# Kernel optimization log

Hardware: AMD Instinct MI355X
Metric: run time of the kernel (lower is better)

The kernel has to match this reference:

```python
import jax, jax.numpy as jnp
import numpy as np

N_SITES = 64   # lattice sites
BOND = 32      # virtual bond dimension D
PHYS = 2       # physical (spin) dimension
BATCH = 32768  # Monte Carlo samples


def spin_to_occupancy(s):
    # spins in {-1,+1} -> physical indices in {0,1}
    return ((s + 1) // 2).astype(jnp.int32)


def setup_inputs() -> dict:
    key = jax.random.key(0)
    k1, k2, k3, k4 = jax.random.split(key, 4)
    # site tensors: boundary sites have bond dim 1, interior sites are (PHYS, D, D)
    t_first = jax.random.uniform(k1, (PHYS, 1, BOND), dtype=jnp.float32)
    t_mid = jax.random.uniform(k2, (N_SITES - 2, PHYS, BOND, BOND), dtype=jnp.float32)
    t_last = jax.random.uniform(k3, (PHYS, BOND, 1), dtype=jnp.float32)
    bits = jax.random.randint(k4, (BATCH, N_SITES), 0, 2)
    x = (2 * bits - 1).astype(jnp.int32)  # spins +-1
    return {"t_first": t_first, "t_mid": t_mid, "t_last": t_last, "x": x}


def reference(t_first, t_mid, t_last, x):
    idx = spin_to_occupancy(x)  # (B, n_sites)
    # first site: left bond = 1, so state = t_first[idx0, 0, :]  (B, D)
    state = t_first[idx[:, 0], 0, :]

    # interior sites: sequential chain of gather + batched mat-vec
    def step(state, xs):
        T, i = xs            # T: (PHYS, D, D), i: (B,)
        mats = T[i]          # (B, D, D) gather by physical index
        return jnp.einsum('bi,bij->bj', state, mats), None

    state, _ = jax.lax.scan(step, state, (t_mid, idx[:, 1:-1].T))

    # last site: right bond = 1
    amps = jnp.einsum('bi,bi->b', state, t_last[idx[:, -1], :, 0])  # (B,)
    return jnp.log(amps)
```

## Files before the change

kernel.cpp:

```cpp
#include <hip/hip_runtime.h>
#include <math.h>

#define N_MID 62
#define NPAIR 31
#define BATCH 32768

typedef float f32x4 __attribute__((ext_vector_type(4)));
typedef unsigned int u32x2 __attribute__((ext_vector_type(2)));
typedef unsigned int u32x4 __attribute__((ext_vector_type(4)));

__device__ __forceinline__ long mklong(unsigned a, unsigned b) {
    u32x2 t = {a, b};
    return __builtin_bit_cast(long, t);
}
__device__ __forceinline__ unsigned pack_fp8x4(float a, float b, float c, float d) {
    int r = __builtin_amdgcn_cvt_pk_fp8_f32(a, b, 0, false);
    r = __builtin_amdgcn_cvt_pk_fp8_f32(c, d, r, true);
    return (unsigned)r;
}

__global__ __launch_bounds__(64) void prefix_kernel(const float* __restrict__ t_mid,
                                                    unsigned* __restrict__ wsP) {
    __shared__ float M1s[1024], M2s[1024];
    const int l = threadIdx.x, q = l >> 4, m = l & 15;
    const int i = blockIdx.x >> 2, v = blockIdx.x & 3;

    const float4* s1 = (const float4*)(t_mid + (size_t)((2 * i) * 2 + (v & 1)) * 1024);
    const float4* s2 = (const float4*)(t_mid + (size_t)((2 * i + 1) * 2 + (v >> 1)) * 1024);
    #pragma unroll
    for (int c = 0; c < 4; ++c) {
        ((float4*)M1s)[c * 64 + l] = s1[c * 64 + l];
        ((float4*)M2s)[c * 64 + l] = s2[c * 64 + l];
    }
    __syncthreads();

    float colv[2][32];
    #pragma unroll
    for (int t = 0; t < 2; ++t)
        #pragma unroll
        for (int mm = 0; mm < 32; ++mm)
            colv[t][mm] = M2s[mm * 32 + 16 * t + m];

    float o0[8], o1[8];
    #pragma unroll
    for (int j = 0; j < 8; ++j) {
        int a = 16 * (j >> 2) + 4 * q + (j & 3);
        float acc0 = 0.f, acc1 = 0.f;
        #pragma unroll
        for (int mm = 0; mm < 32; ++mm) {
            float r = M1s[a * 32 + mm];
            acc0 = fmaf(r, colv[0][mm], acc0);
            acc1 = fmaf(r, colv[1][mm], acc1);
        }
        o0[j] = acc0;
        o1[j] = acc1;
    }

    u32x4 outw;
    outw[0] = pack_fp8x4(o0[0], o0[1], o0[2], o0[3]);
    outw[1] = pack_fp8x4(o0[4], o0[5], o0[6], o0[7]);
    outw[2] = pack_fp8x4(o1[0], o1[1], o1[2], o1[3]);
    outw[3] = pack_fp8x4(o1[4], o1[5], o1[6], o1[7]);
    ((u32x4*)wsP)[blockIdx.x * 64 + l] = outw;
}

__global__ __launch_bounds__(256, 2) void mps_mfma_kernel(
    const float* __restrict__ t_first,
    const float* __restrict__ t_last,
    const int*   __restrict__ x,
    const unsigned* __restrict__ wsP,
    float* __restrict__ out)
{
    const int tid  = threadIdx.x;
    const int w    = tid >> 6;
    const int l    = tid & 63;
    const int q    = l >> 4;
    const int e    = l & 15;
    const int base = (blockIdx.x * 4 + w) * 16;

    unsigned long long mrot;
    {
        const int4* xr = (const int4*)(x + (size_t)(base + e) * 64 + 16 * q);
        unsigned chunk = 0;
        #pragma unroll
        for (int c = 0; c < 4; ++c) {
            int4 vv = xr[c];
            chunk |= (unsigned)(vv.x > 0) << (4 * c + 0);
            chunk |= (unsigned)(vv.y > 0) << (4 * c + 1);
            chunk |= (unsigned)(vv.z > 0) << (4 * c + 2);
            chunk |= (unsigned)(vv.w > 0) << (4 * c + 3);
        }
        unsigned sh = chunk << ((q & 1) * 16);
        unsigned lo = (q < 2) ? sh : 0u;
        unsigned hi = (q >= 2) ? sh : 0u;
        lo |= (unsigned)__shfl_xor((int)lo, 16);
        lo |= (unsigned)__shfl_xor((int)lo, 32);
        hi |= (unsigned)__shfl_xor((int)hi, 16);
        hi |= (unsigned)__shfl_xor((int)hi, 32);
        unsigned long long mask = ((unsigned long long)hi << 32) | lo;
        const float* tf = t_first + ((mask & 1ull) ? 32 : 0);
        mrot = mask >> 1;
        (void)tf;
    }

    float st[8];
    {
        const float* tf = t_first + ((x[(size_t)(base + e) * 64] > 0) ? 32 : 0);
        #pragma unroll
        for (int j = 0; j < 8; ++j)
            st[j] = tf[16 * (j >> 2) + 4 * q + (j & 3)];
    }
    unsigned Bd0 = pack_fp8x4(st[0], st[1], st[2], st[3]);
    unsigned Bd1 = pack_fp8x4(st[4], st[5], st[6], st[7]);

    int expsum = 0;
    const f32x4 cz = {0.f, 0.f, 0.f, 0.f};

    const u32x4* W = (const u32x4*)wsP + l;
    u32x4 Q0[4], Q1[4];
    #pragma unroll
    for (int v = 0; v < 4; ++v) Q0[v] = W[v * 64];
    #pragma unroll
    for (int v = 0; v < 4; ++v) Q1[v] = W[(4 + v) * 64];

    auto step = [&](u32x4* Q, const u32x4* pf) {
        unsigned vl = (unsigned)mrot & 3u;
        mrot >>= 2;

        f32x4 y0 = cz, y1 = cz;
        #pragma unroll
        for (int v = 0; v < 4; ++v) {
            long A0 = mklong(Q[v][0], Q[v][1]);
            long A1 = mklong(Q[v][2], Q[v][3]);
            bool sel = (vl == (unsigned)v);
            long u = mklong(sel ? Bd0 : 0u, sel ? Bd1 : 0u);
            y0 = __builtin_amdgcn_mfma_f32_16x16x32_fp8_fp8(A0, u, y0, 0, 0, 0);
            y1 = __builtin_amdgcn_mfma_f32_16x16x32_fp8_fp8(A1, u, y1, 0, 0, 0);
        }

        if (pf) {
            #pragma unroll
            for (int v = 0; v < 4; ++v) Q[v] = pf[v * 64];
        }

        #pragma unroll
        for (int r = 0; r < 4; ++r) { st[r] = y0[r]; st[4 + r] = y1[r]; }

        float mx = st[0];
        #pragma unroll
        for (int j = 1; j < 8; ++j) mx = fmaxf(mx, st[j]);
        mx = fmaxf(mx, __shfl_xor(mx, 16));
        mx = fmaxf(mx, __shfl_xor(mx, 32));
        int ex = (int)((__float_as_uint(mx) >> 23) & 0xFF) - 127;
        float sc = __uint_as_float((unsigned)(127 - ex) << 23);
        #pragma unroll
        for (int j = 0; j < 8; ++j) st[j] *= sc;
        expsum += ex;

        Bd0 = pack_fp8x4(st[0], st[1], st[2], st[3]);
        Bd1 = pack_fp8x4(st[4], st[5], st[6], st[7]);
    };

    const u32x4* pf = W + 8 * 64;
    for (int k = 0; k < 15; ++k) {
        step(Q0, pf);
        step(Q1, (k < 14) ? pf + 4 * 64 : nullptr);
        pf += 8 * 64;
    }
    step(Q0, nullptr);

    const float* tl = t_last + ((mrot & 1ull) ? 32 : 0);
    float amp = 0.f;
    #pragma unroll
    for (int j = 0; j < 8; ++j)
        amp = fmaf(st[j], tl[16 * (j >> 2) + 4 * q + (j & 3)], amp);
    amp += __shfl_xor(amp, 16);
    amp += __shfl_xor(amp, 32);

    if (l < 16)
        out[base + l] = logf(amp) + 0.69314718055994531f * (float)expsum;
}

extern "C" void kernel_launch(void* const* d_in, const int* in_sizes, int n_in,
                              void* d_out, int out_size, void* d_ws, size_t ws_size,
                              hipStream_t stream) {
    const float* t_first = (const float*)d_in[0];
    const float* t_mid   = (const float*)d_in[1];
    const float* t_last  = (const float*)d_in[2];
    const int*   x       = (const int*)d_in[3];
    float* out           = (float*)d_out;

    unsigned* wsP = (unsigned*)d_ws;

    hipLaunchKernelGGL(prefix_kernel, dim3(NPAIR * 4), dim3(64), 0, stream, t_mid, wsP);
    hipLaunchKernelGGL(mps_mfma_kernel, dim3(BATCH / 64), dim3(256), 0, stream,
                       t_first, t_last, x, wsP, out);
}
```

Baseline: 78.49 us.

## Use 16x16x128 scaled FP8 MFMA per step with permlane-swapped B operand

Each chain step previously issued eight 16x16x32 FP8 MFMAs, four per output half. It now issues two 16x16x128 f8f6f4 scaled MFMAs, with unit scales, by stacking the four two-site variants along K. The prefix kernel writes its output in a layout that matches the new A operand. Each lane gathers the state vector for its variant slot with permlane16/32 swaps, and the max reduction also uses these swaps instead of shuffles. The goal is to shorten the serial dependency chain per step, at the cost of extra cross-lane data movement and a layout that must match exactly.

```diff
diff --git a/kernel.cpp b/kernel.cpp
--- a/kernel.cpp
+++ b/kernel.cpp
@@ -1,28 +1,45 @@
 #include <hip/hip_runtime.h>
 #include <math.h>
 
-#define N_MID 62
 #define NPAIR 31
 #define BATCH 32768
 
 typedef float f32x4 __attribute__((ext_vector_type(4)));
+typedef int   i32x8 __attribute__((ext_vector_type(8)));
 typedef unsigned int u32x2 __attribute__((ext_vector_type(2)));
 typedef unsigned int u32x4 __attribute__((ext_vector_type(4)));
 
-__device__ __forceinline__ long mklong(unsigned a, unsigned b) {
-    u32x2 t = {a, b};
-    return __builtin_bit_cast(long, t);
-}
 __device__ __forceinline__ unsigned pack_fp8x4(float a, float b, float c, float d) {
     int r = __builtin_amdgcn_cvt_pk_fp8_f32(a, b, 0, false);
     r = __builtin_amdgcn_cvt_pk_fp8_f32(c, d, r, true);
     return (unsigned)r;
 }
 
+__device__ __forceinline__ void lane_swap16(unsigned a, unsigned& ev, unsigned& od) {
+#if __has_builtin(__builtin_amdgcn_permlane16_swap)
+    auto r = __builtin_amdgcn_permlane16_swap((int)a, (int)a, false, false);
+    ev = (unsigned)r[0]; od = (unsigned)r[1];
+#else
+    unsigned p = (unsigned)__shfl_xor((int)a, 16);
+    bool hi = (threadIdx.x >> 4) & 1;
+    ev = hi ? p : a; od = hi ? a : p;
+#endif
+}
+__device__ __forceinline__ void lane_swap32(unsigned a, unsigned& lo, unsigned& hi) {
+#if __has_builtin(__builtin_amdgcn_permlane32_swap)
+    auto r = __builtin_amdgcn_permlane32_swap((int)a, (int)a, false, false);
+    lo = (unsigned)r[0]; hi = (unsigned)r[1];
+#else
+    unsigned p = (unsigned)__shfl_xor((int)a, 32);
+    bool up = (threadIdx.x & 32) != 0;
+    lo = up ? p : a; hi = up ? a : p;
+#endif
+}
+
 __global__ __launch_bounds__(64) void prefix_kernel(const float* __restrict__ t_mid,
                                                     unsigned* __restrict__ wsP) {
     __shared__ float M1s[1024], M2s[1024];
-    const int l = threadIdx.x, q = l >> 4, m = l & 15;
+    const int l = threadIdx.x, h = l >> 4, m = l & 15;
     const int i = blockIdx.x >> 2, v = blockIdx.x & 3;
 
     const float4* s1 = (const float4*)(t_mid + (size_t)((2 * i) * 2 + (v & 1)) * 1024);
@@ -44,7 +61,7 @@
     float o0[8], o1[8];
     #pragma unroll
     for (int j = 0; j < 8; ++j) {
-        int a = 16 * (j >> 2) + 4 * q + (j & 3);
+        int a = 16 * (j >> 2) + 4 * h + (j & 3);
         float acc0 = 0.f, acc1 = 0.f;
         #pragma unroll
         for (int mm = 0; mm < 32; ++mm) {
@@ -56,13 +73,57 @@
         o1[j] = acc1;
     }
 
-    u32x4 outw;
-    outw[0] = pack_fp8x4(o0[0], o0[1], o0[2], o0[3]);
-    outw[1] = pack_fp8x4(o0[4], o0[5], o0[6], o0[7]);
-    outw[2] = pack_fp8x4(o1[0], o1[1], o1[2], o1[3]);
-    outw[3] = pack_fp8x4(o1[4], o1[5], o1[6], o1[7]);
-    ((u32x4*)wsP)[blockIdx.x * 64 + l] = outw;
-}
+    unsigned* dst0 = wsP + (((size_t)blockIdx.x * 2 + 0) * 16 + m) * 8 + h * 2;
+    u32x2 w0 = {pack_fp8x4(o0[0], o0[1], o0[2], o0[3]),
+                pack_fp8x4(o0[4], o0[5], o0[6], o0[7])};
+    *(u32x2*)dst0 = w0;
+    unsigned* dst1 = wsP + (((size_t)blockIdx.x * 2 + 1) * 16 + m) * 8 + h * 2;
+    u32x2 w1 = {pack_fp8x4(o1[0], o1[1], o1[2], o1[3]),
+                pack_fp8x4(o1[4], o1[5], o1[6], o1[7])};
+    *(u32x2*)dst1 = w1;
+}
+
+#define MPS_STEP(QQ, PF) do {                                                 \
+    unsigned vl = (unsigned)mrot & 3u; mrot >>= 2;                            \
+    unsigned E0, O0, E1, O1;                                                  \
+    lane_swap16(Bd0, E0, O0); lane_swap16(Bd1, E1, O1);                       \
+    unsigned g0, g1, g2, g3, g4, g5, g6, g7;                                  \
+    lane_swap32(E0, g0, g4); lane_swap32(E1, g1, g5);                         \
+    lane_swap32(O0, g2, g6); lane_swap32(O1, g3, g7);                         \
+    bool selq = (vl == (unsigned)q);                                          \
+    i32x8 Bv;                                                                 \
+    Bv[0] = selq ? (int)g0 : 0; Bv[1] = selq ? (int)g1 : 0;                   \
+    Bv[2] = selq ? (int)g2 : 0; Bv[3] = selq ? (int)g3 : 0;                   \
+    Bv[4] = selq ? (int)g4 : 0; Bv[5] = selq ? (int)g5 : 0;                   \
+    Bv[6] = selq ? (int)g6 : 0; Bv[7] = selq ? (int)g7 : 0;                   \
+    i32x8 A0v, A1v;                                                           \
+    A0v[0]=(int)QQ[0][0]; A0v[1]=(int)QQ[0][1]; A0v[2]=(int)QQ[0][2]; A0v[3]=(int)QQ[0][3]; \
+    A0v[4]=(int)QQ[1][0]; A0v[5]=(int)QQ[1][1]; A0v[6]=(int)QQ[1][2]; A0v[7]=(int)QQ[1][3]; \
+    A1v[0]=(int)QQ[2][0]; A1v[1]=(int)QQ[2][1]; A1v[2]=(int)QQ[2][2]; A1v[3]=(int)QQ[2][3]; \
+    A1v[4]=(int)QQ[3][0]; A1v[5]=(int)QQ[3][1]; A1v[6]=(int)QQ[3][2]; A1v[7]=(int)QQ[3][3]; \
+    const u32x4* pf_ = (PF);                                                  \
+    if (pf_) { QQ[0] = pf_[0]; QQ[1] = pf_[1]; QQ[2] = pf_[32]; QQ[3] = pf_[33]; } \
+    f32x4 y0 = __builtin_amdgcn_mfma_scale_f32_16x16x128_f8f6f4(              \
+        A0v, Bv, cz, 0, 0, 0, 0x7f7f7f7f, 0, 0x7f7f7f7f);                     \
+    f32x4 y1 = __builtin_amdgcn_mfma_scale_f32_16x16x128_f8f6f4(              \
+        A1v, Bv, cz, 0, 0, 0, 0x7f7f7f7f, 0, 0x7f7f7f7f);                     \
+    _Pragma("unroll")                                                         \
+    for (int r = 0; r < 4; ++r) { st[r] = y0[r]; st[4 + r] = y1[r]; }         \
+    float mx = fmaxf(fmaxf(fmaxf(st[0], st[1]), fmaxf(st[2], st[3])),         \
+                     fmaxf(fmaxf(st[4], st[5]), fmaxf(st[6], st[7])));        \
+    { unsigned a_, b_;                                                        \
+      lane_swap16(__float_as_uint(mx), a_, b_);                               \
+      mx = fmaxf(__uint_as_float(a_), __uint_as_float(b_));                   \
+      lane_swap32(__float_as_uint(mx), a_, b_);                               \
+      mx = fmaxf(__uint_as_float(a_), __uint_as_float(b_)); }                 \
+    int ex = (int)((__float_as_uint(mx) >> 23) & 0xFF) - 127;                 \
+    float sc = __uint_as_float((unsigned)(127 - ex) << 23);                   \
+    _Pragma("unroll")                                                         \
+    for (int j = 0; j < 8; ++j) st[j] *= sc;                                  \
+    expsum += ex;                                                             \
+    Bd0 = pack_fp8x4(st[0], st[1], st[2], st[3]);                             \
+    Bd1 = pack_fp8x4(st[4], st[5], st[6], st[7]);                             \
+} while (0)
 
 __global__ __launch_bounds__(256, 2) void mps_mfma_kernel(
     const float* __restrict__ t_first,
@@ -98,9 +159,7 @@
         hi |= (unsigned)__shfl_xor((int)hi, 16);
         hi |= (unsigned)__shfl_xor((int)hi, 32);
         unsigned long long mask = ((unsigned long long)hi << 32) | lo;
-        const float* tf = t_first + ((mask & 1ull) ? 32 : 0);
         mrot = mask >> 1;
-        (void)tf;
     }
 
     float st[8];
@@ -116,58 +175,18 @@
     int expsum = 0;
     const f32x4 cz = {0.f, 0.f, 0.f, 0.f};
 
-    const u32x4* W = (const u32x4*)wsP + l;
+    const u32x4* Wl = (const u32x4*)wsP + (q * 64 + e * 2);
     u32x4 Q0[4], Q1[4];
-    #pragma unroll
-    for (int v = 0; v < 4; ++v) Q0[v] = W[v * 64];
-    #pragma unroll
-    for (int v = 0; v < 4; ++v) Q1[v] = W[(4 + v) * 64];
-
-    auto step = [&](u32x4* Q, const u32x4* pf) {
-        unsigned vl = (unsigned)mrot & 3u;
-        mrot >>= 2;
-
-        f32x4 y0 = cz, y1 = cz;
-        #pragma unroll
-        for (int v = 0; v < 4; ++v) {
-            long A0 = mklong(Q[v][0], Q[v][1]);
-            long A1 = mklong(Q[v][2], Q[v][3]);
-            bool sel = (vl == (unsigned)v);
-            long u = mklong(sel ? Bd0 : 0u, sel ? Bd1 : 0u);
-            y0 = __builtin_amdgcn_mfma_f32_16x16x32_fp8_fp8(A0, u, y0, 0, 0, 0);
-            y1 = __builtin_amdgcn_mfma_f32_16x16x32_fp8_fp8(A1, u, y1, 0, 0, 0);
-        }
-
-        if (pf) {
-            #pragma unroll
-            for (int v = 0; v < 4; ++v) Q[v] = pf[v * 64];
-        }
-
-        #pragma unroll
-        for (int r = 0; r < 4; ++r) { st[r] = y0[r]; st[4 + r] = y1[r]; }
-
-        float mx = st[0];
-        #pragma unroll
-        for (int j = 1; j < 8; ++j) mx = fmaxf(mx, st[j]);
-        mx = fmaxf(mx, __shfl_xor(mx, 16));
-        mx = fmaxf(mx, __shfl_xor(mx, 32));
-        int ex = (int)((__float_as_uint(mx) >> 23) & 0xFF) - 127;
-        float sc = __uint_as_float((unsigned)(127 - ex) << 23);
-        #pragma unroll
-        for (int j = 0; j < 8; ++j) st[j] *= sc;
-        expsum += ex;
-
-        Bd0 = pack_fp8x4(st[0], st[1], st[2], st[3]);
-        Bd1 = pack_fp8x4(st[4], st[5], st[6], st[7]);
-    };
-
-    const u32x4* pf = W + 8 * 64;
+    Q0[0] = Wl[0];   Q0[1] = Wl[1];   Q0[2] = Wl[32];  Q0[3] = Wl[33];
+    Q1[0] = Wl[256]; Q1[1] = Wl[257]; Q1[2] = Wl[288]; Q1[3] = Wl[289];
+
+    const u32x4* pf = Wl + 512;
     for (int k = 0; k < 15; ++k) {
-        step(Q0, pf);
-        step(Q1, (k < 14) ? pf + 4 * 64 : nullptr);
-        pf += 8 * 64;
-    }
-    step(Q0, nullptr);
+        MPS_STEP(Q0, pf);
+        MPS_STEP(Q1, (k < 14) ? (pf + 256) : (const u32x4*)0);
+        pf += 512;
+    }
+    MPS_STEP(Q0, (const u32x4*)0);
 
     const float* tl = t_last + ((mrot & 1ull) ? 32 : 0);
     float amp = 0.f;
```

New measurement: 80.64 us. +2.7%, slower.
